# Performance work log

Hardware: AMD Instinct MI355X
Metric: run time of the kernel (lower is better)

Reference implementation:

```python
import jax, jax.numpy as jnp
import numpy as np

TOP_K = 2  # num_experts_per_tok


def setup_inputs() -> dict:
    key = jax.random.key(0)
    k1, k2, k3, k4, k5 = jax.random.split(key, 5)
    B, S, D, F, E = 2, 1024, 1024, 2048, 8
    return {
        "x": jax.random.normal(k1, (B, S, D), dtype=jnp.float32),
        "router_kernel_DE": jax.random.normal(k2, (D, E), dtype=jnp.float32) * 0.02,
        "kernel_gating_EDF": jax.random.normal(k3, (E, D, F), dtype=jnp.float32) * 0.02,
        "kernel_up_EDF": jax.random.normal(k4, (E, D, F), dtype=jnp.float32) * 0.02,
        "kernel_down_EFD": jax.random.normal(k5, (E, F, D), dtype=jnp.float32) * 0.02,
    }


def reference(x, router_kernel_DE, kernel_gating_EDF, kernel_up_EDF, kernel_down_EFD):
    E = router_kernel_DE.shape[-1]
    x = x.astype(jnp.float32)
    # --- Router ---
    logits_BSE = jnp.einsum('BSD,DE->BSE', x, router_kernel_DE)
    probs_BSE = jax.nn.softmax(logits_BSE.astype(jnp.float32), axis=-1)
    weights_BSK, indices_BSK = jax.lax.top_k(probs_BSE, TOP_K)
    norm_weights_BSK = jax.nn.softmax(weights_BSK, axis=-1)
    # scatter top-k weights into dense [B,S,E]
    one_hot_BSKE = jax.nn.one_hot(indices_BSK, num_classes=E, dtype=x.dtype)
    full_weights_BSE = jnp.sum(one_hot_BSKE * norm_weights_BSK[..., None], axis=2)
    # --- Dense-over-all-experts MoE forward ---
    gating_BSEF = jnp.einsum('BSD,EDF->BSEF', x, kernel_gating_EDF)
    act_BSEF = jax.nn.silu(gating_BSEF)
    up_BSEF = jnp.einsum('BSD,EDF->BSEF', x, kernel_up_EDF)
    fuse_BSEF = act_BSEF * up_BSEF
    down_BSED = jnp.einsum('BSEF,EFD->BSED', fuse_BSEF, kernel_down_EFD)
    out_BSD = jnp.einsum('BSED,BSE->BSD', down_BSED, full_weights_BSE)
    return out_BSD.astype(jnp.float32)
```

## Files before the change

### kernel.cpp

```cpp
#include <hip/hip_runtime.h>
#include <hip/hip_bf16.h>
#include <stdint.h>

#define T_TOK 2048
#define DIM 1024
#define FDIM 2048
#define NEXP 8
#define NSLOT 4096

typedef short bf16x8 __attribute__((ext_vector_type(8)));
typedef float f32x4 __attribute__((ext_vector_type(4)));

__device__ __forceinline__ unsigned short f2bf(float f) {
  union { float f; unsigned int u; } v; v.f = f;
  unsigned int r = v.u + 0x7FFFu + ((v.u >> 16) & 1u);
  return (unsigned short)(r >> 16);
}

__device__ __forceinline__ void gld_lds16(const void* g, void* l) {
  __builtin_amdgcn_global_load_lds(
      (const __attribute__((address_space(1))) unsigned int*)g,
      (__attribute__((address_space(3))) unsigned int*)l, 16, 0, 0);
}

__global__ void router_kernel(const float* __restrict__ x, const float* __restrict__ rk,
                              int* __restrict__ counts, int* __restrict__ tok_e,
                              float* __restrict__ tok_w) {
  int w = threadIdx.x >> 6, lane = threadIdx.x & 63;
  int t = blockIdx.x * 4 + w;
  float acc[NEXP];
#pragma unroll
  for (int e = 0; e < NEXP; ++e) acc[e] = 0.f;
  const float4* xr = (const float4*)(x + (size_t)t * DIM);
#pragma unroll
  for (int i = 0; i < 4; ++i) {
    float4 xv = xr[i * 64 + lane];
    int d0 = (i * 64 + lane) * 4;
#pragma unroll
    for (int j = 0; j < 4; ++j) {
      const float4* rr = (const float4*)(rk + (size_t)(d0 + j) * NEXP);
      float4 r0 = rr[0], r1 = rr[1];
      float xs = (j == 0) ? xv.x : (j == 1) ? xv.y : (j == 2) ? xv.z : xv.w;
      acc[0] += xs * r0.x; acc[1] += xs * r0.y; acc[2] += xs * r0.z; acc[3] += xs * r0.w;
      acc[4] += xs * r1.x; acc[5] += xs * r1.y; acc[6] += xs * r1.z; acc[7] += xs * r1.w;
    }
  }
#pragma unroll
  for (int off = 32; off > 0; off >>= 1) {
#pragma unroll
    for (int e = 0; e < NEXP; ++e) acc[e] += __shfl_xor(acc[e], off, 64);
  }
  if (lane == 0) {
    float m = acc[0];
    for (int e = 1; e < NEXP; ++e) m = fmaxf(m, acc[e]);
    float p[NEXP], s = 0.f;
    for (int e = 0; e < NEXP; ++e) { p[e] = expf(acc[e] - m); s += p[e]; }
    float inv = 1.f / s;
    for (int e = 0; e < NEXP; ++e) p[e] *= inv;
    int i1 = 0;
    for (int e = 1; e < NEXP; ++e) if (p[e] > p[i1]) i1 = e;
    int i2 = (i1 == 0) ? 1 : 0;
    for (int e = 0; e < NEXP; ++e) if (e != i1 && p[e] > p[i2]) i2 = e;
    float e1 = expf(p[i1]), e2 = expf(p[i2]);
    float winv = 1.f / (e1 + e2);
    tok_e[t * 2] = i1; tok_e[t * 2 + 1] = i2;
    tok_w[t * 2] = e1 * winv; tok_w[t * 2 + 1] = e2 * winv;
    atomicAdd(&counts[i1], 1); atomicAdd(&counts[i2], 1);
  }
}

__global__ void scan_kernel(const int* __restrict__ counts, int* __restrict__ offsets) {
  if (threadIdx.x == 0) {
    int s = 0;
    for (int e = 0; e < NEXP; ++e) { offsets[e] = s; s += counts[e]; }
  }
}

__global__ void assign_kernel(const int* __restrict__ tok_e, const float* __restrict__ tok_w,
                              const int* __restrict__ offsets, int* __restrict__ cursor,
                              int* __restrict__ slot_token, float* __restrict__ slot_weight,
                              int* __restrict__ tok_slot) {
  int t = blockIdx.x * 256 + threadIdx.x;
  if (t >= T_TOK) return;
#pragma unroll
  for (int k = 0; k < 2; ++k) {
    int e = tok_e[t * 2 + k];
    int pos = atomicAdd(&cursor[e], 1);
    int slot = offsets[e] + pos;
    slot_token[slot] = t;
    slot_weight[slot] = tok_w[t * 2 + k];
    tok_slot[t * 2 + k] = slot;
  }
}

__global__ void cvt_x_kernel(const float* __restrict__ x, unsigned short* __restrict__ xb) {
  int i = blockIdx.x * 256 + threadIdx.x;
  const float4* p = (const float4*)x;
  float4 a = p[i * 2], b = p[i * 2 + 1];
  uint4 o;
  o.x = ((unsigned)f2bf(a.y) << 16) | f2bf(a.x);
  o.y = ((unsigned)f2bf(a.w) << 16) | f2bf(a.z);
  o.z = ((unsigned)f2bf(b.y) << 16) | f2bf(b.x);
  o.w = ((unsigned)f2bf(b.w) << 16) | f2bf(b.z);
  ((uint4*)xb)[i] = o;
}

__global__ void transpose_cvt_kernel(const float* __restrict__ in, unsigned short* __restrict__ out,
                                     int R, int C) {
  __shared__ float lds[64][65];
  int e = blockIdx.z;
  size_t base = (size_t)e * (size_t)R * (size_t)C;
  int rb = blockIdx.y * 64, cb = blockIdx.x * 64;
  int tid = threadIdx.x;
  int col4 = (tid & 15) * 4, row = tid >> 4;
#pragma unroll
  for (int it = 0; it < 4; ++it) {
    int r = row + it * 16;
    float4 v = *(const float4*)(in + base + (size_t)(rb + r) * C + cb + col4);
    lds[col4 + 0][r] = v.x; lds[col4 + 1][r] = v.y;
    lds[col4 + 2][r] = v.z; lds[col4 + 3][r] = v.w;
  }
  __syncthreads();
  int r2 = (tid & 31) * 2, c = tid >> 5;
#pragma unroll
  for (int it = 0; it < 8; ++it) {
    int cc = c + it * 8;
    unsigned v = ((unsigned)f2bf(lds[cc][r2 + 1]) << 16) | f2bf(lds[cc][r2]);
    *(unsigned*)(out + base + (size_t)(cb + cc) * R + rb + r2) = v;
  }
}


__global__ __launch_bounds__(256) void gemm_gateup(
    const unsigned short* __restrict__ xb, const unsigned short* __restrict__ wg,
    const unsigned short* __restrict__ wu, const int* __restrict__ counts,
    const int* __restrict__ offsets, const int* __restrict__ slot_token,
    unsigned short* __restrict__ fuse) {
  int e = blockIdx.z;
  int cnt = counts[e];
  int mt = blockIdx.y;
  if (mt * 128 >= cnt) return;
  int off = offsets[e];
  int nt = blockIdx.x;
  __shared__ unsigned short Al[128 * 64];
  __shared__ unsigned short Bgl[128 * 64];
  __shared__ unsigned short Bul[128 * 64];
  int tid = threadIdx.x, w = tid >> 6, lane = tid & 63;
  int w4 = w * 4;
  int csrc = ((lane & 7) ^ (lane >> 3)) * 8;
  const unsigned short* asrc[4];
  const unsigned short* bgsrc[4];
  const unsigned short* busrc[4];
#pragma unroll
  for (int ii = 0; ii < 4; ++ii) {
    int i = w4 + ii;
    int r = i * 8 + (lane >> 3);
    int row = mt * 128 + r;
    int tok = (row < cnt) ? slot_token[off + row] : 0;
    asrc[ii] = xb + (size_t)tok * DIM + csrc;
    size_t frow = (size_t)e * FDIM + (size_t)(nt * 128 + r);
    bgsrc[ii] = wg + frow * DIM + csrc;
    busrc[ii] = wu + frow * DIM + csrc;
  }
  f32x4 accg[4][4] = {};
  f32x4 accu[4][4] = {};
  int wr = (w >> 1) * 64, wc = (w & 1) * 64;
  int swz = (lane & 7) << 3;
  int kof0 = ((lane >> 4) * 8) ^ swz;
  int kof1 = (32 + (lane >> 4) * 8) ^ swz;
  for (int k0 = 0; k0 < DIM; k0 += 64) {
#pragma unroll
    for (int ii = 0; ii < 4; ++ii) {
      int i = w4 + ii;
      gld_lds16(asrc[ii] + k0, &Al[i * 512]);
      gld_lds16(bgsrc[ii] + k0, &Bgl[i * 512]);
      gld_lds16(busrc[ii] + k0, &Bul[i * 512]);
    }
    __syncthreads();
#pragma unroll
    for (int kk = 0; kk < 2; ++kk) {
      int kof = kk ? kof1 : kof0;
      bf16x8 af[4], bg[4], bu[4];
#pragma unroll
      for (int q = 0; q < 4; ++q) {
        af[q] = *(const bf16x8*)&Al[(wr + q * 16 + (lane & 15)) * 64 + kof];
        bg[q] = *(const bf16x8*)&Bgl[(wc + q * 16 + (lane & 15)) * 64 + kof];
        bu[q] = *(const bf16x8*)&Bul[(wc + q * 16 + (lane & 15)) * 64 + kof];
      }
#pragma unroll
      for (int m4 = 0; m4 < 4; ++m4) {
#pragma unroll
        for (int n4 = 0; n4 < 4; ++n4) {
          accg[m4][n4] = __builtin_amdgcn_mfma_f32_16x16x32_bf16(af[m4], bg[n4], accg[m4][n4], 0, 0, 0);
          accu[m4][n4] = __builtin_amdgcn_mfma_f32_16x16x32_bf16(af[m4], bu[n4], accu[m4][n4], 0, 0, 0);
        }
      }
    }
    __syncthreads();
  }
#pragma unroll
  for (int m4 = 0; m4 < 4; ++m4) {
#pragma unroll
    for (int n4 = 0; n4 < 4; ++n4) {
      f32x4 g = accg[m4][n4], u = accu[m4][n4];
#pragma unroll
      for (int j = 0; j < 4; ++j) {
        int r = wr + m4 * 16 + (lane >> 4) * 4 + j;
        int row = mt * 128 + r;
        if (row < cnt) {
          float gv = g[j];
          float val = gv / (1.f + expf(-gv)) * u[j];
          int f = nt * 128 + wc + n4 * 16 + (lane & 15);
          fuse[(size_t)(off + row) * FDIM + f] = f2bf(val);
        }
      }
    }
  }
}

__global__ __launch_bounds__(256) void gemm_down(
    const unsigned short* __restrict__ fuse, const unsigned short* __restrict__ wd,
    const int* __restrict__ counts, const int* __restrict__ offsets,
    const float* __restrict__ slot_weight, float* __restrict__ part) {
  int e = blockIdx.z;
  int cnt = counts[e];
  int mt = blockIdx.y;
  if (mt * 128 >= cnt) return;
  int off = offsets[e];
  int nt = blockIdx.x;
  __shared__ unsigned short Al[128 * 64];
  __shared__ unsigned short Bl[128 * 64];
  int tid = threadIdx.x, w = tid >> 6, lane = tid & 63;
  int w4 = w * 4;
  int csrc = ((lane & 7) ^ (lane >> 3)) * 8;
  const unsigned short* asrc[4];
  const unsigned short* bsrc[4];
#pragma unroll
  for (int ii = 0; ii < 4; ++ii) {
    int i = w4 + ii;
    int r = i * 8 + (lane >> 3);
    int row = mt * 128 + r;
    int grow = (row < cnt) ? (off + row) : off;
    asrc[ii] = fuse + (size_t)grow * FDIM + csrc;
    size_t drow = (size_t)e * DIM + (size_t)(nt * 128 + r);
    bsrc[ii] = wd + drow * FDIM + csrc;
  }
  f32x4 acc[4][4] = {};
  int wr = (w >> 1) * 64, wc = (w & 1) * 64;
  int swz = (lane & 7) << 3;
  int kof0 = ((lane >> 4) * 8) ^ swz;
  int kof1 = (32 + (lane >> 4) * 8) ^ swz;
  for (int k0 = 0; k0 < FDIM; k0 += 64) {
#pragma unroll
    for (int ii = 0; ii < 4; ++ii) {
      int i = w4 + ii;
      gld_lds16(asrc[ii] + k0, &Al[i * 512]);
      gld_lds16(bsrc[ii] + k0, &Bl[i * 512]);
    }
    __syncthreads();
#pragma unroll
    for (int kk = 0; kk < 2; ++kk) {
      int kof = kk ? kof1 : kof0;
      bf16x8 af[4], bfr[4];
#pragma unroll
      for (int q = 0; q < 4; ++q) {
        af[q] = *(const bf16x8*)&Al[(wr + q * 16 + (lane & 15)) * 64 + kof];
        bfr[q] = *(const bf16x8*)&Bl[(wc + q * 16 + (lane & 15)) * 64 + kof];
      }
#pragma unroll
      for (int m4 = 0; m4 < 4; ++m4) {
#pragma unroll
        for (int n4 = 0; n4 < 4; ++n4) {
          acc[m4][n4] = __builtin_amdgcn_mfma_f32_16x16x32_bf16(af[m4], bfr[n4], acc[m4][n4], 0, 0, 0);
        }
      }
    }
    __syncthreads();
  }
#pragma unroll
  for (int m4 = 0; m4 < 4; ++m4) {
#pragma unroll
    for (int j = 0; j < 4; ++j) {
      int r = wr + m4 * 16 + (lane >> 4) * 4 + j;
      int row = mt * 128 + r;
      if (row < cnt) {
        float wgt = slot_weight[off + row];
#pragma unroll
        for (int n4 = 0; n4 < 4; ++n4) {
          int d = nt * 128 + wc + n4 * 16 + (lane & 15);
          part[(size_t)(off + row) * DIM + d] = acc[m4][n4][j] * wgt;
        }
      }
    }
  }
}

__global__ void combine_kernel(const float* __restrict__ part, const int* __restrict__ tok_slot,
                               float* __restrict__ out) {
  int i = blockIdx.x * 256 + threadIdx.x;
  int t = i >> 8;
  int c = i & 255;
  int s0 = tok_slot[t * 2], s1 = tok_slot[t * 2 + 1];
  float4 a = ((const float4*)(part + (size_t)s0 * DIM))[c];
  float4 b = ((const float4*)(part + (size_t)s1 * DIM))[c];
  float4 o;
  o.x = a.x + b.x; o.y = a.y + b.y; o.z = a.z + b.z; o.w = a.w + b.w;
  ((float4*)(out + (size_t)t * DIM))[c] = o;
}

extern "C" void kernel_launch(void* const* d_in, const int* in_sizes, int n_in,
                              void* d_out, int out_size, void* d_ws, size_t ws_size,
                              hipStream_t stream) {
  (void)in_sizes; (void)n_in; (void)out_size;
  const float* x    = (const float*)d_in[0];
  const float* rk   = (const float*)d_in[1];
  const float* wg_f = (const float*)d_in[2];
  const float* wu_f = (const float*)d_in[3];
  const float* wd_f = (const float*)d_in[4];
  float* out = (float*)d_out;

  char* ws = (char*)d_ws;
  size_t o_xb   = 0;
  size_t o_wg   = o_xb + (size_t)T_TOK * DIM * 2;
  size_t o_wu   = o_wg + (size_t)NEXP * FDIM * DIM * 2;
  size_t o_wd   = o_wu + (size_t)NEXP * FDIM * DIM * 2;
  size_t o_fuse = o_wd + (size_t)NEXP * DIM * FDIM * 2;
  size_t o_part = o_fuse + (size_t)NSLOT * FDIM * 2;
  size_t o_meta = o_part + (size_t)NSLOT * DIM * 4;
  size_t o_counts = o_meta;
  size_t o_cursor = o_counts + 32;
  size_t o_offs   = o_cursor + 32;
  size_t o_tok_e  = o_offs + 32;
  size_t o_tok_w  = o_tok_e + (size_t)T_TOK * 2 * 4;
  size_t o_tok_s  = o_tok_w + (size_t)T_TOK * 2 * 4;
  size_t o_st     = o_tok_s + (size_t)T_TOK * 2 * 4;
  size_t o_sw     = o_st + (size_t)NSLOT * 4;
  size_t need     = o_sw + (size_t)NSLOT * 4;
  if (ws_size < need) return;

  unsigned short* xb   = (unsigned short*)(ws + o_xb);
  unsigned short* wgt  = (unsigned short*)(ws + o_wg);
  unsigned short* wut  = (unsigned short*)(ws + o_wu);
  unsigned short* wdt  = (unsigned short*)(ws + o_wd);
  unsigned short* fuse = (unsigned short*)(ws + o_fuse);
  float* part          = (float*)(ws + o_part);
  int* counts          = (int*)(ws + o_counts);
  int* cursor          = (int*)(ws + o_cursor);
  int* offsets         = (int*)(ws + o_offs);
  int* tok_e           = (int*)(ws + o_tok_e);
  float* tok_w         = (float*)(ws + o_tok_w);
  int* tok_slot        = (int*)(ws + o_tok_s);
  int* slot_token      = (int*)(ws + o_st);
  float* slot_weight   = (float*)(ws + o_sw);

  hipMemsetAsync(ws + o_counts, 0, 64, stream);
  router_kernel<<<T_TOK / 4, 256, 0, stream>>>(x, rk, counts, tok_e, tok_w);
  scan_kernel<<<1, 64, 0, stream>>>(counts, offsets);
  assign_kernel<<<T_TOK / 256, 256, 0, stream>>>(tok_e, tok_w, offsets, cursor,
                                                 slot_token, slot_weight, tok_slot);
  cvt_x_kernel<<<(T_TOK * DIM / 8) / 256, 256, 0, stream>>>(x, xb);
  transpose_cvt_kernel<<<dim3(FDIM / 64, DIM / 64, NEXP), 256, 0, stream>>>(wg_f, wgt, DIM, FDIM);
  transpose_cvt_kernel<<<dim3(FDIM / 64, DIM / 64, NEXP), 256, 0, stream>>>(wu_f, wut, DIM, FDIM);
  transpose_cvt_kernel<<<dim3(DIM / 64, FDIM / 64, NEXP), 256, 0, stream>>>(wd_f, wdt, FDIM, DIM);
  gemm_gateup<<<dim3(FDIM / 128, 16, NEXP), 256, 0, stream>>>(xb, wgt, wut, counts, offsets,
                                                              slot_token, fuse);
  gemm_down<<<dim3(DIM / 128, 16, NEXP), 256, 0, stream>>>(fuse, wdt, counts, offsets,
                                                           slot_weight, part);
  combine_kernel<<<(T_TOK * DIM / 4) / 256, 256, 0, stream>>>(part, tok_slot, out);
}
```

Measured before the change: 288.1 us.

## Double-buffer LDS tiles in gate/up and down GEMMs to overlap loads with MFMA

Both expert GEMM kernels now keep two LDS buffers per operand. The next K-tile is issued with global_load_lds while the MFMAs run on the current tile, which removes the load-then-wait stall at each K step. This doubles LDS use (96KB for gate/up, 64KB for down), which may lower occupancy. The loop is also fully unrolled, which adds code size.

```diff
diff --git a/kernel.cpp b/kernel.cpp
--- a/kernel.cpp
+++ b/kernel.cpp
@@ -142,9 +142,9 @@
   if (mt * 128 >= cnt) return;
   int off = offsets[e];
   int nt = blockIdx.x;
-  __shared__ unsigned short Al[128 * 64];
-  __shared__ unsigned short Bgl[128 * 64];
-  __shared__ unsigned short Bul[128 * 64];
+  __shared__ unsigned short Al[2][128 * 64];
+  __shared__ unsigned short Bgl[2][128 * 64];
+  __shared__ unsigned short Bul[2][128 * 64];
   int tid = threadIdx.x, w = tid >> 6, lane = tid & 63;
   int w4 = w * 4;
   int csrc = ((lane & 7) ^ (lane >> 3)) * 8;
@@ -168,24 +168,26 @@
   int swz = (lane & 7) << 3;
   int kof0 = ((lane >> 4) * 8) ^ swz;
   int kof1 = (32 + (lane >> 4) * 8) ^ swz;
-  for (int k0 = 0; k0 < DIM; k0 += 64) {
+
+  auto stage = [&](int buf, int k0) {
 #pragma unroll
     for (int ii = 0; ii < 4; ++ii) {
       int i = w4 + ii;
-      gld_lds16(asrc[ii] + k0, &Al[i * 512]);
-      gld_lds16(bgsrc[ii] + k0, &Bgl[i * 512]);
-      gld_lds16(busrc[ii] + k0, &Bul[i * 512]);
-    }
-    __syncthreads();
+      gld_lds16(asrc[ii] + k0, &Al[buf][i * 512]);
+      gld_lds16(bgsrc[ii] + k0, &Bgl[buf][i * 512]);
+      gld_lds16(busrc[ii] + k0, &Bul[buf][i * 512]);
+    }
+  };
+  auto compute = [&](int buf) {
 #pragma unroll
     for (int kk = 0; kk < 2; ++kk) {
       int kof = kk ? kof1 : kof0;
       bf16x8 af[4], bg[4], bu[4];
 #pragma unroll
       for (int q = 0; q < 4; ++q) {
-        af[q] = *(const bf16x8*)&Al[(wr + q * 16 + (lane & 15)) * 64 + kof];
-        bg[q] = *(const bf16x8*)&Bgl[(wc + q * 16 + (lane & 15)) * 64 + kof];
-        bu[q] = *(const bf16x8*)&Bul[(wc + q * 16 + (lane & 15)) * 64 + kof];
+        af[q] = *(const bf16x8*)&Al[buf][(wr + q * 16 + (lane & 15)) * 64 + kof];
+        bg[q] = *(const bf16x8*)&Bgl[buf][(wc + q * 16 + (lane & 15)) * 64 + kof];
+        bu[q] = *(const bf16x8*)&Bul[buf][(wc + q * 16 + (lane & 15)) * 64 + kof];
       }
 #pragma unroll
       for (int m4 = 0; m4 < 4; ++m4) {
@@ -196,8 +198,20 @@
         }
       }
     }
+  };
+
+  stage(0, 0);
+  __syncthreads();
+#pragma unroll
+  for (int k0 = 0; k0 < DIM; k0 += 128) {
+    stage(1, k0 + 64);
+    compute(0);
     __syncthreads();
-  }
+    if (k0 + 128 < DIM) stage(0, k0 + 128);
+    compute(1);
+    __syncthreads();
+  }
+
 #pragma unroll
   for (int m4 = 0; m4 < 4; ++m4) {
 #pragma unroll
@@ -228,8 +242,8 @@
   if (mt * 128 >= cnt) return;
   int off = offsets[e];
   int nt = blockIdx.x;
-  __shared__ unsigned short Al[128 * 64];
-  __shared__ unsigned short Bl[128 * 64];
+  __shared__ unsigned short Al[2][128 * 64];
+  __shared__ unsigned short Bl[2][128 * 64];
   int tid = threadIdx.x, w = tid >> 6, lane = tid & 63;
   int w4 = w * 4;
   int csrc = ((lane & 7) ^ (lane >> 3)) * 8;
@@ -250,22 +264,24 @@
   int swz = (lane & 7) << 3;
   int kof0 = ((lane >> 4) * 8) ^ swz;
   int kof1 = (32 + (lane >> 4) * 8) ^ swz;
-  for (int k0 = 0; k0 < FDIM; k0 += 64) {
+
+  auto stage = [&](int buf, int k0) {
 #pragma unroll
     for (int ii = 0; ii < 4; ++ii) {
       int i = w4 + ii;
-      gld_lds16(asrc[ii] + k0, &Al[i * 512]);
-      gld_lds16(bsrc[ii] + k0, &Bl[i * 512]);
-    }
-    __syncthreads();
+      gld_lds16(asrc[ii] + k0, &Al[buf][i * 512]);
+      gld_lds16(bsrc[ii] + k0, &Bl[buf][i * 512]);
+    }
+  };
+  auto compute = [&](int buf) {
 #pragma unroll
     for (int kk = 0; kk < 2; ++kk) {
       int kof = kk ? kof1 : kof0;
       bf16x8 af[4], bfr[4];
 #pragma unroll
       for (int q = 0; q < 4; ++q) {
-        af[q] = *(const bf16x8*)&Al[(wr + q * 16 + (lane & 15)) * 64 + kof];
-        bfr[q] = *(const bf16x8*)&Bl[(wc + q * 16 + (lane & 15)) * 64 + kof];
+        af[q] = *(const bf16x8*)&Al[buf][(wr + q * 16 + (lane & 15)) * 64 + kof];
+        bfr[q] = *(const bf16x8*)&Bl[buf][(wc + q * 16 + (lane & 15)) * 64 + kof];
       }
 #pragma unroll
       for (int m4 = 0; m4 < 4; ++m4) {
@@ -275,8 +291,20 @@
         }
       }
     }
+  };
+
+  stage(0, 0);
+  __syncthreads();
+#pragma unroll
+  for (int k0 = 0; k0 < FDIM; k0 += 128) {
+    stage(1, k0 + 64);
+    compute(0);
     __syncthreads();
-  }
+    if (k0 + 128 < FDIM) stage(0, k0 + 128);
+    compute(1);
+    __syncthreads();
+  }
+
 #pragma unroll
   for (int m4 = 0; m4 < 4; ++m4) {
 #pragma unroll
```

Result: slower. 293.9 us (+2.0%).
